# Kernel tuning notes

Hardware: AMD Instinct MI355X
Metric: run time of the kernel (lower is better)

Reference implementation:

```python
import jax, jax.numpy as jnp
import numpy as np

N = 30000
E = 480000
D_IN = 128
EPS = 1e-5
NEG_SLOPE = 0.2
# (in_dim, out_channels, heads) per GATConv layer; concat=True everywhere (PyG default)
CFG = [(D_IN, 100, 5), (500, 50, 5), (250, 32, 4), (128, 8, 4), (32, 1, 1)]
BN_DIMS = (500, 250, 128)


def setup_inputs() -> dict:
    key = jax.random.key(0)
    ks = iter(jax.random.split(key, 80))
    inp = {
        "x": jax.random.normal(next(ks), (N, D_IN), jnp.float32),
        "edge_index": jax.random.randint(next(ks), (2, E), 0, N),
        "edge_weight": jax.random.uniform(next(ks), (E, 1), jnp.float32),
    }
    for l, (cin, cout, h) in enumerate(CFG, 1):
        s = 1.0 / np.sqrt(cin)
        inp[f"W{l}"] = jax.random.normal(next(ks), (cin, h * cout), jnp.float32) * s
        inp[f"a_s{l}"] = jax.random.normal(next(ks), (1, h, cout), jnp.float32) * 0.1
        inp[f"a_d{l}"] = jax.random.normal(next(ks), (1, h, cout), jnp.float32) * 0.1
        inp[f"We{l}"] = jax.random.normal(next(ks), (1, h * cout), jnp.float32)
        inp[f"a_e{l}"] = jax.random.normal(next(ks), (1, h, cout), jnp.float32) * 0.1
        inp[f"b{l}"] = jnp.zeros((h * cout,), jnp.float32)
    for l, d in zip((1, 2, 3), BN_DIMS):
        inp[f"g{l}"] = jnp.ones((d,), jnp.float32)
        inp[f"beta{l}"] = jnp.zeros((d,), jnp.float32)
    return inp


def _gat(x, src, dst, ea, W, a_s, a_d, We, a_e, b, heads, cout):
    """PyG GATConv with edge_dim attention (concat=True)."""
    n = x.shape[0]
    h = (x @ W).reshape(n, heads, cout)            # [N,H,C]
    e = (ea @ We).reshape(-1, heads, cout)         # [E,H,C]
    al_src = (h * a_s).sum(-1)                     # [N,H]
    al_dst = (h * a_d).sum(-1)                     # [N,H]
    logit = jax.nn.leaky_relu(al_src[src] + al_dst[dst] + (e * a_e).sum(-1), NEG_SLOPE)
    m = jax.ops.segment_max(logit, dst, num_segments=n)
    m = jnp.where(jnp.isfinite(m), m, 0.0)
    ex = jnp.exp(logit - m[dst])                   # [E,H]
    den = jax.ops.segment_sum(ex, dst, num_segments=n)
    alpha = ex / jnp.maximum(den[dst], 1e-16)      # segment softmax over in-edges of dst
    out = jax.ops.segment_sum(h[src] * alpha[..., None], dst, num_segments=n)
    return out.reshape(n, heads * cout) + b


def _bn(x, g, b):
    mu = x.mean(0)
    var = x.var(0)  # biased, as torch uses for normalization
    return (x - mu) * jax.lax.rsqrt(var + EPS) * g + b


def reference(x, edge_index, edge_weight,
              W1, a_s1, a_d1, We1, a_e1, b1,
              W2, a_s2, a_d2, We2, a_e2, b2,
              W3, a_s3, a_d3, We3, a_e3, b3,
              W4, a_s4, a_d4, We4, a_e4, b4,
              W5, a_s5, a_d5, We5, a_e5, b5,
              g1, beta1, g2, beta2, g3, beta3):
    # add self loops (PyG default) with edge_attr fill_value='mean'
    loop = jnp.arange(N)
    src = jnp.concatenate([edge_index[0], loop])
    dst = jnp.concatenate([edge_index[1], loop])
    ea = jnp.concatenate([edge_weight, jnp.full((N, 1), edge_weight.mean(), edge_weight.dtype)], axis=0)

    h = _gat(x, src, dst, ea, W1, a_s1, a_d1, We1, a_e1, b1, 5, 100)
    h = jax.nn.relu(_bn(h, g1, beta1))
    h = _gat(h, src, dst, ea, W2, a_s2, a_d2, We2, a_e2, b2, 5, 50)
    h = jax.nn.relu(_bn(h, g2, beta2))
    h = _gat(h, src, dst, ea, W3, a_s3, a_d3, We3, a_e3, b3, 4, 32)
    h = jax.nn.relu(_bn(h, g3, beta3))
    h = _gat(h, src, dst, ea, W4, a_s4, a_d4, We4, a_e4, b4, 4, 8)
    h = jax.nn.relu(h)
    h = _gat(h, src, dst, ea, W5, a_s5, a_d5, We5, a_e5, b5, 1, 1)
    return h
```

## Files before the change

### kernel.cpp

```cpp
#include <hip/hip_runtime.h>
#include <hip/hip_bf16.h>
#include <math.h>

#define NN 30000
#define EE 480000
#define ET (EE + NN)
#define NEG_SLOPE 0.2f
#define BN_EPS 1e-5f

struct LayerCfg { int cin, C, H; };
static const LayerCfg g_cfg[5] = {
    {128, 100, 5}, {500, 50, 5}, {250, 32, 4}, {128, 8, 4}, {32, 1, 1}
};

typedef short short8 __attribute__((ext_vector_type(8)));
typedef float f32x4 __attribute__((ext_vector_type(4)));

__device__ __forceinline__ unsigned short f2bf(float f) {
    unsigned int u = __builtin_bit_cast(unsigned int, f);
    u = (u + 0x7FFFu + ((u >> 16) & 1u)) >> 16;
    return (unsigned short)u;
}
__device__ __forceinline__ float bf2f(unsigned short h) {
    unsigned int u = ((unsigned int)h) << 16;
    return __builtin_bit_cast(float, u);
}


__global__ void ewsum_kernel(const float* __restrict__ ew, float* __restrict__ out) {
    __shared__ float sdata[256];
    int tid = threadIdx.x;
    float s = 0.f;
    for (int i = blockIdx.x * blockDim.x + tid; i < EE; i += gridDim.x * blockDim.x)
        s += ew[i];
    sdata[tid] = s;
    __syncthreads();
    for (int off = 128; off > 0; off >>= 1) {
        if (tid < off) sdata[tid] += sdata[tid + off];
        __syncthreads();
    }
    if (tid == 0) atomicAdd(out, sdata[0]);
}

__global__ void build_edges_kernel(const int* __restrict__ ei,
                                   int* __restrict__ rank, int* __restrict__ cnt) {
    int e = blockIdx.x * blockDim.x + threadIdx.x;
    if (e >= ET) return;
    int d = (e < EE) ? ei[EE + e] : (e - EE);
    rank[e] = atomicAdd(&cnt[d], 1);
}

__global__ void scan_kernel(const int* __restrict__ cnt, int* __restrict__ off) {
    __shared__ int lsum[1024];
    const int T = 1024;
    int t = threadIdx.x;
    int chunk = (NN + T - 1) / T;
    int base = t * chunk;
    int end = min(NN, base + chunk);
    int s = 0;
    for (int i = base; i < end; i++) s += cnt[i];
    lsum[t] = s;
    __syncthreads();
    for (int d = 1; d < T; d <<= 1) {
        int v = (t >= d) ? lsum[t - d] : 0;
        __syncthreads();
        lsum[t] += v;
        __syncthreads();
    }
    int run = (t == 0) ? 0 : lsum[t - 1];
    for (int i = base; i < end; i++) {
        off[i] = run;
        run += cnt[i];
    }
    if (t == 0) off[NN] = ET;
}

__global__ void fill_kernel(const int* __restrict__ ei, const int* __restrict__ rank,
                            const float* __restrict__ ew, const float* __restrict__ esum,
                            const int* __restrict__ off,
                            int* __restrict__ csr_src, float* __restrict__ csr_ea) {
    int e = blockIdx.x * blockDim.x + threadIdx.x;
    if (e >= ET) return;
    int sv, d;
    if (e < EE) { sv = ei[e]; d = ei[EE + e]; }
    else        { sv = e - EE; d = e - EE; }
    int p = off[d] + rank[e];
    csr_src[p] = sv;
    csr_ea[p]  = (e < EE) ? ew[e] : esum[0] * (1.0f / (float)EE);
}


struct PrepArgs {
    const float* W[5];
    const float* We[5];
    const float* ae[5];
    unsigned short* bh[5];
    unsigned short* bl[5];
    float* wedot;
    int K[5], N[5], Kp[5], Np[5], C[5], H[5];
};

__global__ void transpose_all_kernel(PrepArgs a) {
    int l = blockIdx.z;
    if (blockIdx.x == 0 && blockIdx.y == 0 && threadIdx.y == 0 && threadIdx.x < 8) {
        int hd = threadIdx.x;
        if (hd < a.H[l]) {
            int C = a.C[l];
            const float* We = a.We[l] + hd * C;
            const float* ae = a.ae[l] + hd * C;
            float s = 0.f;
            for (int c = 0; c < C; c++) s += We[c] * ae[c];
            a.wedot[l * 8 + hd] = s;
        }
    }
    int Kp = a.Kp[l], Np = a.Np[l], K = a.K[l], N = a.N[l];
    int kb = blockIdx.x * 32, nb = blockIdx.y * 32;
    if (kb >= Kp || nb >= Np) return;
    const float* B = a.W[l];
    unsigned short* Bth = a.bh[l];
    unsigned short* Btl = a.bl[l];
    __shared__ float tile[32][33];
    int tx = threadIdx.x, ty = threadIdx.y;
#pragma unroll
    for (int i = 0; i < 4; i++) {
        int k = kb + ty + i * 8, n = nb + tx;
        tile[ty + i * 8][tx] = (k < K && n < N) ? B[(size_t)k * N + n] : 0.f;
    }
    __syncthreads();
#pragma unroll
    for (int i = 0; i < 4; i++) {
        int n = nb + ty + i * 8, k = kb + tx;
        if (n < Np && k < Kp) {
            float v = tile[tx][ty + i * 8];
            unsigned short hi = f2bf(v);
            unsigned short lo = f2bf(v - bf2f(hi));
            size_t idx = (size_t)n * Kp + k;
            Bth[idx] = hi;
            Btl[idx] = lo;
        }
    }
}

#define GBM 128
#define GBNT 128
#define GBK 32
#define ASTR 36
__global__ __launch_bounds__(256) void gemm_split_kernel(const float* __restrict__ A,
                                                         const unsigned short* __restrict__ Bt_hi,
                                                         const unsigned short* __restrict__ Bt_lo,
                                                         float* __restrict__ Cm,
                                                         unsigned short* __restrict__ Ch16,
                                                         int M, int Kp, int Nc,
                                                         const float* __restrict__ colsum,
                                                         const float* __restrict__ colsumsq,
                                                         const float* __restrict__ g,
                                                         const float* __restrict__ beta,
                                                         int D) {
    __shared__ short AsH[GBM * ASTR];
    __shared__ short AsL[GBM * ASTR];
    __shared__ short BsH[GBNT * ASTR];
    __shared__ short BsL[GBNT * ASTR];
    __shared__ float sscale[512];
    __shared__ float sshift[512];
    int tid = threadIdx.x;
    bool bn = (colsum != nullptr);
    if (bn) {
        for (int c = tid; c < Kp; c += 256) {
            float sc = 0.f, sh = 0.f;
            if (c < D) {
                float mu = colsum[c] * (1.0f / (float)NN);
                float var = colsumsq[c] * (1.0f / (float)NN) - mu * mu;
                sc = g[c] * rsqrtf(var + BN_EPS);
                sh = beta[c] - mu * sc;
            }
            sscale[c] = sc;
            sshift[c] = sh;
        }
        __syncthreads();
    }
    int wave = tid >> 6, lane = tid & 63;
    int q = lane >> 4, r = lane & 15;
    int m0 = blockIdx.y * GBM, n0 = blockIdx.x * GBNT;
    int wm = (wave & 1) * 64, wn = (wave >> 1) * 64;
    f32x4 acc[4][4];
#pragma unroll
    for (int i = 0; i < 4; i++)
#pragma unroll
        for (int j = 0; j < 4; j++) acc[i][j] = (f32x4)(0.f);

    int arow2 = tid >> 1;
    int acol2 = (tid & 1) * 16;
    int brow = tid >> 2;
    int bcol = (tid & 3) * 8;

    int ksteps = Kp / GBK;
    for (int ks = 0; ks < ksteps; ks++) {
        int k0 = ks * GBK;
        {
            int m = m0 + arow2;
            float v[16];
            if (m < M) {
                const float* Ap = A + (size_t)m * Kp + k0 + acol2;
                float4 f0 = *(const float4*)(Ap);
                float4 f1 = *(const float4*)(Ap + 4);
                float4 f2 = *(const float4*)(Ap + 8);
                float4 f3 = *(const float4*)(Ap + 12);
                v[0]=f0.x; v[1]=f0.y; v[2]=f0.z; v[3]=f0.w;
                v[4]=f1.x; v[5]=f1.y; v[6]=f1.z; v[7]=f1.w;
                v[8]=f2.x; v[9]=f2.y; v[10]=f2.z; v[11]=f2.w;
                v[12]=f3.x; v[13]=f3.y; v[14]=f3.z; v[15]=f3.w;
                if (bn) {
                    int cb = k0 + acol2;
#pragma unroll
                    for (int i = 0; i < 16; i++)
                        v[i] = fmaxf(v[i] * sscale[cb + i] + sshift[cb + i], 0.f);
                }
            } else {
#pragma unroll
                for (int i = 0; i < 16; i++) v[i] = 0.f;
            }
#pragma unroll
            for (int i = 0; i < 16; i++) {
                unsigned short hi = f2bf(v[i]);
                unsigned short lo = f2bf(v[i] - bf2f(hi));
                AsH[arow2 * ASTR + acol2 + i] = (short)hi;
                AsL[arow2 * ASTR + acol2 + i] = (short)lo;
            }
        }
#pragma unroll
        for (int p = 0; p < 2; p++) {
            int row = p * 64 + brow;
            size_t gidx = (size_t)(n0 + row) * Kp + k0 + bcol;
            *((uint4*)(BsH + row * ASTR + bcol)) = *((const uint4*)(Bt_hi + gidx));
            *((uint4*)(BsL + row * ASTR + bcol)) = *((const uint4*)(Bt_lo + gidx));
        }
        __syncthreads();
        short8 ah[4], al[4], bh[4], bl[4];
#pragma unroll
        for (int i = 0; i < 4; i++) {
            ah[i] = *((const short8*)(AsH + (wm + i * 16 + r) * ASTR + q * 8));
            al[i] = *((const short8*)(AsL + (wm + i * 16 + r) * ASTR + q * 8));
        }
#pragma unroll
        for (int j = 0; j < 4; j++) {
            bh[j] = *((const short8*)(BsH + (wn + j * 16 + r) * ASTR + q * 8));
            bl[j] = *((const short8*)(BsL + (wn + j * 16 + r) * ASTR + q * 8));
        }
#pragma unroll
        for (int i = 0; i < 4; i++)
#pragma unroll
            for (int j = 0; j < 4; j++) {
                acc[i][j] = __builtin_amdgcn_mfma_f32_16x16x32_bf16(ah[i], bh[j], acc[i][j], 0, 0, 0);
                acc[i][j] = __builtin_amdgcn_mfma_f32_16x16x32_bf16(ah[i], bl[j], acc[i][j], 0, 0, 0);
                acc[i][j] = __builtin_amdgcn_mfma_f32_16x16x32_bf16(al[i], bh[j], acc[i][j], 0, 0, 0);
            }
        __syncthreads();
    }
#pragma unroll
    for (int i = 0; i < 4; i++) {
#pragma unroll
        for (int j = 0; j < 4; j++) {
#pragma unroll
            for (int reg = 0; reg < 4; reg++) {
                int mrow = m0 + wm + i * 16 + q * 4 + reg;
                int ncol = n0 + wn + j * 16 + r;
                if (mrow < M && ncol < Nc) {
                    float val = acc[i][j][reg];
                    if (Cm)   Cm[(size_t)mrow * Nc + ncol] = val;
                    if (Ch16) Ch16[(size_t)mrow * Nc + ncol] = f2bf(val);
                }
            }
        }
    }
}

__global__ void gemv_l5_kernel(const float* __restrict__ X, const float* __restrict__ W,
                               const float* __restrict__ a_s, const float* __restrict__ a_d,
                               float* __restrict__ h, float* __restrict__ al_src,
                               float* __restrict__ al_dst) {
    __shared__ float w[32];
    if (threadIdx.x < 32) w[threadIdx.x] = W[threadIdx.x];
    __syncthreads();
    int n = blockIdx.x * blockDim.x + threadIdx.x;
    if (n >= NN) return;
    const float* row = X + (size_t)n * 32;
    float s = 0.f;
#pragma unroll
    for (int i = 0; i < 8; i++) {
        float4 f = *(const float4*)(row + i * 4);
        s += f.x * w[i * 4] + f.y * w[i * 4 + 1] + f.z * w[i * 4 + 2] + f.w * w[i * 4 + 3];
    }
    h[n] = s;
    al_src[n] = s * a_s[0];
    al_dst[n] = s * a_d[0];
}

__global__ void al_wave_h16_kernel(const unsigned short* __restrict__ h16,
                                   const float* __restrict__ a_s,
                                   const float* __restrict__ a_d,
                                   float* __restrict__ al_src, float* __restrict__ al_dst,
                                   int H, int C, int HC) {
    int w = (blockIdx.x * blockDim.x + threadIdx.x) >> 6;
    int lane = threadIdx.x & 63;
    if (w >= NN) return;
    const unsigned short* row = h16 + (size_t)w * HC;
    float s1[5] = {0.f, 0.f, 0.f, 0.f, 0.f};
    float s2[5] = {0.f, 0.f, 0.f, 0.f, 0.f};
#pragma unroll
    for (int hd = 0; hd < 5; hd++) {
        if (hd >= H) break;
        int base = hd * C;
        for (int c = lane * 2; c < C; c += 128) {
            unsigned int u = *(const unsigned int*)(row + base + c);
            float v0 = bf2f((unsigned short)(u & 0xffffu));
            float v1 = bf2f((unsigned short)(u >> 16));
            s1[hd] += v0 * a_s[base + c] + v1 * a_s[base + c + 1];
            s2[hd] += v0 * a_d[base + c] + v1 * a_d[base + c + 1];
        }
    }
#pragma unroll
    for (int hd = 0; hd < 5; hd++) {
        if (hd >= H) break;
#pragma unroll
        for (int off = 32; off > 0; off >>= 1) {
            s1[hd] += __shfl_xor(s1[hd], off, 64);
            s2[hd] += __shfl_xor(s2[hd], off, 64);
        }
    }
    if (lane == 0) {
#pragma unroll
        for (int hd = 0; hd < 5; hd++) {
            if (hd >= H) break;
            al_src[(size_t)w * H + hd] = s1[hd];
            al_dst[(size_t)w * H + hd] = s2[hd];
        }
    }
}

__global__ void attn_kernel(const float* __restrict__ al_src,
                            const float* __restrict__ al_dst,
                            const int* __restrict__ csr_src,
                            const float* __restrict__ csr_ea,
                            const float* __restrict__ we_dot,
                            const int* __restrict__ off,
                            float* __restrict__ alpha_t, int H, int NH) {
    int t = blockIdx.x * blockDim.x + threadIdx.x;
    if (t >= NH) return;
    int n = t / H, hd = t - n * H;
    int s = off[n], e = off[n + 1];
    float ad = al_dst[(size_t)n * H + hd];
    float wd = we_dot[hd];
    float* arow = alpha_t + (size_t)hd * ET;
    float m = -INFINITY, l = 0.f;
    int p = s;
    for (; p + 3 < e; p += 4) {
        int s0 = csr_src[p], s1 = csr_src[p + 1], s2 = csr_src[p + 2], s3 = csr_src[p + 3];
        float w0 = csr_ea[p], w1 = csr_ea[p + 1], w2 = csr_ea[p + 2], w3 = csr_ea[p + 3];
        float l0 = al_src[(size_t)s0 * H + hd] + ad + w0 * wd;
        float l1 = al_src[(size_t)s1 * H + hd] + ad + w1 * wd;
        float l2 = al_src[(size_t)s2 * H + hd] + ad + w2 * wd;
        float l3 = al_src[(size_t)s3 * H + hd] + ad + w3 * wd;
        l0 = (l0 >= 0.f) ? l0 : NEG_SLOPE * l0;
        l1 = (l1 >= 0.f) ? l1 : NEG_SLOPE * l1;
        l2 = (l2 >= 0.f) ? l2 : NEG_SLOPE * l2;
        l3 = (l3 >= 0.f) ? l3 : NEG_SLOPE * l3;
        arow[p] = l0; arow[p + 1] = l1; arow[p + 2] = l2; arow[p + 3] = l3;
        float mq = fmaxf(fmaxf(l0, l1), fmaxf(l2, l3));
        float nm = fmaxf(m, mq);
        l = l * __expf(m - nm)
          + __expf(l0 - nm) + __expf(l1 - nm) + __expf(l2 - nm) + __expf(l3 - nm);
        m = nm;
    }
    for (; p < e; p++) {
        float lg = al_src[(size_t)csr_src[p] * H + hd] + ad + csr_ea[p] * wd;
        lg = (lg >= 0.f) ? lg : NEG_SLOPE * lg;
        arow[p] = lg;
        float nm = fmaxf(m, lg);
        l = l * __expf(m - nm) + __expf(lg - nm);
        m = nm;
    }
    float inv = 1.f / fmaxf(l, 1e-16f);
    for (p = s; p < e; p++) arow[p] = __expf(arow[p] - m) * inv;
}

__global__ void aggregate_v4h_kernel(const unsigned short* __restrict__ h16,
                                     const float* __restrict__ alpha_t,
                                     const int* __restrict__ off,
                                     const int* __restrict__ csr_src,
                                     const float* __restrict__ bias,
                                     float* __restrict__ out,
                                     int C, int HC, int HC4, int total4, int relu, int opitch) {
    int t = blockIdx.x * blockDim.x + threadIdx.x;
    if (t >= total4) return;
    int n = t / HC4, j4 = t - n * HC4;
    int j = j4 * 4;
    int hd = j / C;
    const float* arow = alpha_t + (size_t)hd * ET;
    int s = off[n], e = off[n + 1];
    float4 acc = make_float4(0.f, 0.f, 0.f, 0.f);
    int p = s;
    for (; p + 3 < e; p += 4) {
        int idx[4]; float a[4];
#pragma unroll
        for (int u = 0; u < 4; u++) { idx[u] = csr_src[p + u]; a[u] = arow[p + u]; }
#pragma unroll
        for (int u = 0; u < 4; u++) {
            ushort4 uv = *(const ushort4*)(h16 + (size_t)idx[u] * HC + j);
            acc.x += a[u] * bf2f(uv.x);
            acc.y += a[u] * bf2f(uv.y);
            acc.z += a[u] * bf2f(uv.z);
            acc.w += a[u] * bf2f(uv.w);
        }
    }
    for (; p < e; p++) {
        int s0 = csr_src[p];
        float a0 = arow[p];
        ushort4 uv = *(const ushort4*)(h16 + (size_t)s0 * HC + j);
        acc.x += a0 * bf2f(uv.x);
        acc.y += a0 * bf2f(uv.y);
        acc.z += a0 * bf2f(uv.z);
        acc.w += a0 * bf2f(uv.w);
    }
    float4 bi = *(const float4*)(bias + j);
    float4 rr = make_float4(acc.x + bi.x, acc.y + bi.y, acc.z + bi.z, acc.w + bi.w);
    if (relu) {
        rr.x = fmaxf(rr.x, 0.f); rr.y = fmaxf(rr.y, 0.f);
        rr.z = fmaxf(rr.z, 0.f); rr.w = fmaxf(rr.w, 0.f);
    }
    *(float4*)(out + (size_t)n * opitch + j) = rr;
}

__global__ void aggregate_v2h_kernel(const unsigned short* __restrict__ h16,
                                     const float* __restrict__ alpha_t,
                                     const int* __restrict__ off,
                                     const int* __restrict__ csr_src,
                                     const float* __restrict__ bias,
                                     float* __restrict__ out,
                                     int C, int HC, int HC2, int total2, int opitch) {
    int t = blockIdx.x * blockDim.x + threadIdx.x;
    if (t >= total2) return;
    int n = t / HC2, j2 = t - n * HC2;
    int j = j2 * 2;
    int hd = j / C;
    const float* arow = alpha_t + (size_t)hd * ET;
    int s = off[n], e = off[n + 1];
    float2 acc = make_float2(0.f, 0.f);
    int p = s;
    for (; p + 3 < e; p += 4) {
        int idx[4]; float a[4];
#pragma unroll
        for (int u = 0; u < 4; u++) { idx[u] = csr_src[p + u]; a[u] = arow[p + u]; }
#pragma unroll
        for (int u = 0; u < 4; u++) {
            ushort2 uv = *(const ushort2*)(h16 + (size_t)idx[u] * HC + j);
            acc.x += a[u] * bf2f(uv.x);
            acc.y += a[u] * bf2f(uv.y);
        }
    }
    for (; p < e; p++) {
        int s0 = csr_src[p];
        float a0 = arow[p];
        ushort2 uv = *(const ushort2*)(h16 + (size_t)s0 * HC + j);
        acc.x += a0 * bf2f(uv.x);
        acc.y += a0 * bf2f(uv.y);
    }
    float2 bi = *(const float2*)(bias + j);
    *(float2*)(out + (size_t)n * opitch + j) = make_float2(acc.x + bi.x, acc.y + bi.y);
}

__global__ void aggregate_kernel(const float* __restrict__ hfeat,
                                 const float* __restrict__ alpha_t,
                                 const int* __restrict__ off, const int* __restrict__ csr_src,
                                 const float* __restrict__ bias, float* __restrict__ out,
                                 int total) {
    int t = blockIdx.x * blockDim.x + threadIdx.x;
    if (t >= total) return;
    int n = t;
    int s = off[n], e = off[n + 1];
    float acc = 0.f;
    int p = s;
    for (; p + 3 < e; p += 4) {
        acc += alpha_t[p] * hfeat[csr_src[p]]
             + alpha_t[p + 1] * hfeat[csr_src[p + 1]]
             + alpha_t[p + 2] * hfeat[csr_src[p + 2]]
             + alpha_t[p + 3] * hfeat[csr_src[p + 3]];
    }
    for (; p < e; p++) acc += alpha_t[p] * hfeat[csr_src[p]];
    out[n] = acc + bias[0];
}


__global__ void bn_stats_kernel(const float* __restrict__ x, float* __restrict__ colsum,
                                float* __restrict__ colsumsq, int D, int pitch) {
    int rows_per_block = (NN + gridDim.x - 1) / gridDim.x;
    int r0 = blockIdx.x * rows_per_block;
    int r1 = min(NN, r0 + rows_per_block);
    int c0 = threadIdx.x;
    int c1 = threadIdx.x + 256;
    float s0 = 0.f, q0 = 0.f, s1 = 0.f, q1 = 0.f;
    for (int r = r0; r < r1; r++) {
        const float* row = x + (size_t)r * pitch;
        if (c0 < D) { float v = row[c0]; s0 += v; q0 += v * v; }
        if (c1 < D) { float v = row[c1]; s1 += v; q1 += v * v; }
    }
    if (c0 < D) { atomicAdd(&colsum[c0], s0); atomicAdd(&colsumsq[c0], q0); }
    if (c1 < D) { atomicAdd(&colsum[c1], s1); atomicAdd(&colsumsq[c1], q1); }
}


static inline size_t align_up(size_t v, size_t a) { return (v + a - 1) / a * a; }

extern "C" void kernel_launch(void* const* d_in, const int* in_sizes, int n_in,
                              void* d_out, int out_size, void* d_ws, size_t ws_size,
                              hipStream_t stream) {
    const float* x_in = (const float*)d_in[0];
    const int* ei     = (const int*)d_in[1];
    const float* ew   = (const float*)d_in[2];

    char* pws = (char*)d_ws;
    size_t off_b = 0;
    auto alloc = [&](size_t bytes) -> void* {
        void* rp = pws + off_b;
        off_b = align_up(off_b + bytes, 256);
        return rp;
    };
    float* B0      = (float*)alloc((size_t)NN * 4);
    float* B1      = (float*)alloc((size_t)NN * 512 * 4);
    unsigned short* H16 = (unsigned short*)alloc((size_t)NN * 500 * 2);
    float* alpha_t = (float*)alloc((size_t)ET * 5 * 4);
    unsigned short* Wt_hi = (unsigned short*)alloc((size_t)600 * 512 * 2);
    unsigned short* Wt_lo = (unsigned short*)alloc((size_t)600 * 512 * 2);
    float* al_src  = (float*)alloc((size_t)NN * 5 * 4);
    float* al_dst  = (float*)alloc((size_t)NN * 5 * 4);
    float* csr_ea  = (float*)alloc((size_t)ET * 4);
    int* rankb     = (int*)alloc((size_t)ET * 4);
    int* csr_src   = (int*)alloc((size_t)ET * 4);
    int* offarr    = (int*)alloc((size_t)(NN + 1) * 4);
    float* we_dot  = (float*)alloc(40 * 4);
    float* esum    = (float*)alloc(4);
    int* cnt       = (int*)alloc((size_t)NN * 4);
    float* colsum_all   = (float*)alloc(3 * 512 * 4);
    float* colsumsq_all = (float*)alloc(3 * 512 * 4);
    char* zero_end = pws + off_b;
    (void)ws_size; (void)n_in; (void)in_sizes; (void)out_size;

    int Kp[5], Np[5];
    size_t wtoff[5];
    size_t acc_off = 0;
    for (int l = 0; l < 5; l++) {
        int K = g_cfg[l].cin, HC = g_cfg[l].C * g_cfg[l].H;
        Kp[l] = (K + 31) / 32 * 32;
        Np[l] = (HC + 127) / 128 * 128;
        wtoff[l] = acc_off;
        acc_off += (size_t)Kp[l] * Np[l];
    }

    PrepArgs pa;
    for (int l = 0; l < 5; l++) {
        pa.W[l]  = (const float*)d_in[3 + l * 6 + 0];
        pa.We[l] = (const float*)d_in[3 + l * 6 + 3];
        pa.ae[l] = (const float*)d_in[3 + l * 6 + 4];
        pa.bh[l] = Wt_hi + wtoff[l];
        pa.bl[l] = Wt_lo + wtoff[l];
        pa.K[l] = g_cfg[l].cin;
        pa.N[l] = g_cfg[l].C * g_cfg[l].H;
        pa.Kp[l] = Kp[l];
        pa.Np[l] = Np[l];
        pa.C[l] = g_cfg[l].C;
        pa.H[l] = g_cfg[l].H;
    }
    pa.wedot = we_dot;

    hipMemsetAsync(esum, 0, (size_t)(zero_end - (char*)esum), stream);
    int ebl = (ET + 255) / 256;
    ewsum_kernel<<<256, 256, 0, stream>>>(ew, esum);
    build_edges_kernel<<<ebl, 256, 0, stream>>>(ei, rankb, cnt);
    scan_kernel<<<1, 1024, 0, stream>>>(cnt, offarr);
    fill_kernel<<<ebl, 256, 0, stream>>>(ei, rankb, ew, esum, offarr, csr_src, csr_ea);

    transpose_all_kernel<<<dim3(16, 16, 5), dim3(32, 8), 0, stream>>>(pa);

    for (int l = 0; l < 5; l++) {
        const LayerCfg& cf = g_cfg[l];
        int H = cf.H, C = cf.C;
        int HC = H * C;
        const float* a_s = (const float*)d_in[3 + l * 6 + 1];
        const float* a_d = (const float*)d_in[3 + l * 6 + 2];
        const float* b   = (const float*)d_in[3 + l * 6 + 5];

        const float* X = (l == 0) ? x_in : B1;
        float* outbuf = (l == 4) ? (float*)d_out : B1;
        int opitch = (l == 4) ? 1 : Kp[l + 1];
        int NH = NN * H;
        int alblocks = (NN * 64 + 255) / 256;

        if (l == 4) {
            gemv_l5_kernel<<<(NN + 255) / 256, 256, 0, stream>>>(
                X, pa.W[4], a_s, a_d, B0, al_src, al_dst);
        } else {
            const float* cs = (l >= 1) ? colsum_all + (l - 1) * 512 : nullptr;
            const float* cq = (l >= 1) ? colsumsq_all + (l - 1) * 512 : nullptr;
            const float* gg = (l >= 1) ? (const float*)d_in[33 + (l - 1) * 2 + 0] : nullptr;
            const float* bb = (l >= 1) ? (const float*)d_in[33 + (l - 1) * 2 + 1] : nullptr;
            int Din = (l >= 1) ? g_cfg[l - 1].C * g_cfg[l - 1].H : 0;
            dim3 ggrid(Np[l] / GBNT, (NN + GBM - 1) / GBM);
            gemm_split_kernel<<<ggrid, 256, 0, stream>>>(X, Wt_hi + wtoff[l], Wt_lo + wtoff[l],
                                                         nullptr, H16,
                                                         NN, Kp[l], HC, cs, cq, gg, bb, Din);
            al_wave_h16_kernel<<<alblocks, 256, 0, stream>>>(H16, a_s, a_d, al_src, al_dst, H, C, HC);
        }

        attn_kernel<<<(NH + 255) / 256, 256, 0, stream>>>(al_src, al_dst, csr_src, csr_ea,
                                                          we_dot + l * 8, offarr, alpha_t, H, NH);

        if (l == 4) {
            aggregate_kernel<<<(NN + 255) / 256, 256, 0, stream>>>(
                B0, alpha_t, offarr, csr_src, b, outbuf, NN);
        } else if ((C & 3) == 0) {
            int HC4 = HC / 4;
            int total4 = NN * HC4;
            aggregate_v4h_kernel<<<(total4 + 255) / 256, 256, 0, stream>>>(
                H16, alpha_t, offarr, csr_src, b, outbuf, C, HC, HC4, total4,
                (l == 3) ? 1 : 0, opitch);
        } else {
            int HC2 = HC / 2;
            int total2 = NN * HC2;
            aggregate_v2h_kernel<<<(total2 + 255) / 256, 256, 0, stream>>>(
                H16, alpha_t, offarr, csr_src, b, outbuf, C, HC, HC2, total2, opitch);
        }

        if (l < 3) {
            bn_stats_kernel<<<512, 256, 0, stream>>>(outbuf, colsum_all + l * 512,
                                                     colsumsq_all + l * 512, HC, opitch);
        }
    }
}
```

Baseline: 826.0 us.

## Pad bf16 feature rows to multiples of 8, vectorize aggregation, fuse prep kernels

Pads the bf16 hidden-feature row pitch to a multiple of 8 so that aggregation can load 16-byte vectors of 8 channels per gathered neighbor. This replaces the separate 4-wide and 2-wide aggregate kernels with one 8-wide kernel that can straddle a head boundary by selecting per-channel alphas. It also merges edge counting, edge-weight summation and weight transpose into one launch to cut launch overhead. The cost is extra padded memory, extra alpha loads per edge, and per-channel select logic in the inner loop. The padded output columns rely on the downstream pitch being large enough to hold them.

Result: no change. 830.6 us (+0.6%).

```diff
diff --git a/kernel.cpp b/kernel.cpp
--- a/kernel.cpp
+++ b/kernel.cpp
@@ -14,6 +14,7 @@
 };
 
 typedef short short8 __attribute__((ext_vector_type(8)));
+typedef unsigned short u16x8 __attribute__((ext_vector_type(8)));
 typedef float f32x4 __attribute__((ext_vector_type(4)));
 
 __device__ __forceinline__ unsigned short f2bf(float f) {
@@ -27,27 +28,87 @@
 }
 
 
-__global__ void ewsum_kernel(const float* __restrict__ ew, float* __restrict__ out) {
+struct PrepArgs {
+    const float* W[5];
+    const float* We[5];
+    const float* ae[5];
+    unsigned short* bh[5];
+    unsigned short* bl[5];
+    float* wedot;
+    int K[5], N[5], Kp[5], Np[5], C[5], H[5];
+};
+
+static const int EBLK = (ET + 255) / 256;
+
+__global__ void prep_fused_kernel(const int* __restrict__ ei, int* __restrict__ rank,
+                                  int* __restrict__ cnt, const float* __restrict__ ew,
+                                  float* __restrict__ esum, PrepArgs a) {
     __shared__ float sdata[256];
+    __shared__ float tile[32][33];
+    int b = blockIdx.x;
     int tid = threadIdx.x;
-    float s = 0.f;
-    for (int i = blockIdx.x * blockDim.x + tid; i < EE; i += gridDim.x * blockDim.x)
-        s += ew[i];
-    sdata[tid] = s;
+
+    if (b < EBLK) {
+        int e = b * 256 + tid;
+        if (e < ET) {
+            int d = (e < EE) ? ei[EE + e] : (e - EE);
+            rank[e] = atomicAdd(&cnt[d], 1);
+        }
+        return;
+    }
+    b -= EBLK;
+    if (b < 256) {
+        float s = 0.f;
+        for (int i = b * 256 + tid; i < EE; i += 65536)
+            s += ew[i];
+        sdata[tid] = s;
+        __syncthreads();
+        for (int off = 128; off > 0; off >>= 1) {
+            if (tid < off) sdata[tid] += sdata[tid + off];
+            __syncthreads();
+        }
+        if (tid == 0) atomicAdd(esum, sdata[0]);
+        return;
+    }
+    b -= 256;
+    int bx = b & 15, by = (b >> 4) & 15, bz = b >> 8;
+    int l = bz;
+    int tx = tid & 31, ty = tid >> 5;
+    if (bx == 0 && by == 0 && ty == 0 && tx < 8) {
+        int hd = tx;
+        if (hd < a.H[l]) {
+            int C = a.C[l];
+            const float* We = a.We[l] + hd * C;
+            const float* ae = a.ae[l] + hd * C;
+            float s = 0.f;
+            for (int c = 0; c < C; c++) s += We[c] * ae[c];
+            a.wedot[l * 8 + hd] = s;
+        }
+    }
+    int Kp = a.Kp[l], Np = a.Np[l], K = a.K[l], N = a.N[l];
+    int kb = bx * 32, nb = by * 32;
+    if (kb >= Kp || nb >= Np) return;
+    const float* B = a.W[l];
+    unsigned short* Bth = a.bh[l];
+    unsigned short* Btl = a.bl[l];
+#pragma unroll
+    for (int i = 0; i < 4; i++) {
+        int k = kb + ty + i * 8, n = nb + tx;
+        tile[ty + i * 8][tx] = (k < K && n < N) ? B[(size_t)k * N + n] : 0.f;
+    }
     __syncthreads();
-    for (int off = 128; off > 0; off >>= 1) {
-        if (tid < off) sdata[tid] += sdata[tid + off];
-        __syncthreads();
-    }
-    if (tid == 0) atomicAdd(out, sdata[0]);
-}
-
-__global__ void build_edges_kernel(const int* __restrict__ ei,
-                                   int* __restrict__ rank, int* __restrict__ cnt) {
-    int e = blockIdx.x * blockDim.x + threadIdx.x;
-    if (e >= ET) return;
-    int d = (e < EE) ? ei[EE + e] : (e - EE);
-    rank[e] = atomicAdd(&cnt[d], 1);
+#pragma unroll
+    for (int i = 0; i < 4; i++) {
+        int n = nb + ty + i * 8, k = kb + tx;
+        if (n < Np && k < Kp) {
+            float v = tile[tx][ty + i * 8];
+            unsigned short hi = f2bf(v);
+            unsigned short lo = f2bf(v - bf2f(hi));
+            size_t idx = (size_t)n * Kp + k;
+            Bth[idx] = hi;
+            Btl[idx] = lo;
+        }
+    }
 }
 
 __global__ void scan_kernel(const int* __restrict__ cnt, int* __restrict__ off) {
@@ -87,58 +148,6 @@
     int p = off[d] + rank[e];
     csr_src[p] = sv;
     csr_ea[p]  = (e < EE) ? ew[e] : esum[0] * (1.0f / (float)EE);
-}
-
-
-struct PrepArgs {
-    const float* W[5];
-    const float* We[5];
-    const float* ae[5];
-    unsigned short* bh[5];
-    unsigned short* bl[5];
-    float* wedot;
-    int K[5], N[5], Kp[5], Np[5], C[5], H[5];
-};
-
-__global__ void transpose_all_kernel(PrepArgs a) {
-    int l = blockIdx.z;
-    if (blockIdx.x == 0 && blockIdx.y == 0 && threadIdx.y == 0 && threadIdx.x < 8) {
-        int hd = threadIdx.x;
-        if (hd < a.H[l]) {
-            int C = a.C[l];
-            const float* We = a.We[l] + hd * C;
-            const float* ae = a.ae[l] + hd * C;
-            float s = 0.f;
-            for (int c = 0; c < C; c++) s += We[c] * ae[c];
-            a.wedot[l * 8 + hd] = s;
-        }
-    }
-    int Kp = a.Kp[l], Np = a.Np[l], K = a.K[l], N = a.N[l];
-    int kb = blockIdx.x * 32, nb = blockIdx.y * 32;
-    if (kb >= Kp || nb >= Np) return;
-    const float* B = a.W[l];
-    unsigned short* Bth = a.bh[l];
-    unsigned short* Btl = a.bl[l];
-    __shared__ float tile[32][33];
-    int tx = threadIdx.x, ty = threadIdx.y;
-#pragma unroll
-    for (int i = 0; i < 4; i++) {
-        int k = kb + ty + i * 8, n = nb + tx;
-        tile[ty + i * 8][tx] = (k < K && n < N) ? B[(size_t)k * N + n] : 0.f;
-    }
-    __syncthreads();
-#pragma unroll
-    for (int i = 0; i < 4; i++) {
-        int n = nb + ty + i * 8, k = kb + tx;
-        if (n < Np && k < Kp) {
-            float v = tile[tx][ty + i * 8];
-            unsigned short hi = f2bf(v);
-            unsigned short lo = f2bf(v - bf2f(hi));
-            size_t idx = (size_t)n * Kp + k;
-            Bth[idx] = hi;
-            Btl[idx] = lo;
-        }
-    }
 }
 
 #define GBM 128
@@ -299,11 +308,11 @@
                                    const float* __restrict__ a_s,
                                    const float* __restrict__ a_d,
                                    float* __restrict__ al_src, float* __restrict__ al_dst,
-                                   int H, int C, int HC) {
+                                   int H, int C, int HCp) {
     int w = (blockIdx.x * blockDim.x + threadIdx.x) >> 6;
     int lane = threadIdx.x & 63;
     if (w >= NN) return;
-    const unsigned short* row = h16 + (size_t)w * HC;
+    const unsigned short* row = h16 + (size_t)w * HCp;
     float s1[5] = {0.f, 0.f, 0.f, 0.f, 0.f};
     float s2[5] = {0.f, 0.f, 0.f, 0.f, 0.f};
 #pragma unroll
@@ -383,89 +392,71 @@
     for (p = s; p < e; p++) arow[p] = __expf(arow[p] - m) * inv;
 }
 
-__global__ void aggregate_v4h_kernel(const unsigned short* __restrict__ h16,
+__global__ void aggregate_v8h_kernel(const unsigned short* __restrict__ h16,
                                      const float* __restrict__ alpha_t,
                                      const int* __restrict__ off,
                                      const int* __restrict__ csr_src,
                                      const float* __restrict__ bias,
                                      float* __restrict__ out,
-                                     int C, int HC, int HC4, int total4, int relu, int opitch) {
+                                     int C, int H, int HC, int hp, int hp8,
+                                     int total8, int relu, int opitch) {
     int t = blockIdx.x * blockDim.x + threadIdx.x;
-    if (t >= total4) return;
-    int n = t / HC4, j4 = t - n * HC4;
-    int j = j4 * 4;
-    int hd = j / C;
-    const float* arow = alpha_t + (size_t)hd * ET;
+    if (t >= total8) return;
+    int n = t / hp8, j8 = t - n * hp8;
+    int j = j8 * 8;
+    int hdA = j / C;
+    int hdB = (j + 7) / C;
+    int bnd = (hdA + 1) * C - j;
+    bnd = (bnd > 8) ? 8 : bnd;
+    float mA = (hdA < H) ? 1.f : 0.f;
+    float mB = (hdB < H) ? 1.f : 0.f;
+    const float* arA = alpha_t + (size_t)((hdA < H) ? hdA : 0) * ET;
+    const float* arB = alpha_t + (size_t)((hdB < H) ? hdB : 0) * ET;
     int s = off[n], e = off[n + 1];
-    float4 acc = make_float4(0.f, 0.f, 0.f, 0.f);
+    const unsigned short* hb = h16 + j;
+    float acc[8];
+#pragma unroll
+    for (int c = 0; c < 8; c++) acc[c] = 0.f;
     int p = s;
     for (; p + 3 < e; p += 4) {
-        int idx[4]; float a[4];
-#pragma unroll
-        for (int u = 0; u < 4; u++) { idx[u] = csr_src[p + u]; a[u] = arow[p + u]; }
+        int idx[4]; float aA[4], aB[4];
 #pragma unroll
         for (int u = 0; u < 4; u++) {
-            ushort4 uv = *(const ushort4*)(h16 + (size_t)idx[u] * HC + j);
-            acc.x += a[u] * bf2f(uv.x);
-            acc.y += a[u] * bf2f(uv.y);
-            acc.z += a[u] * bf2f(uv.z);
-            acc.w += a[u] * bf2f(uv.w);
+            idx[u] = csr_src[p + u];
+            aA[u] = arA[p + u];
+            aB[u] = arB[p + u];
+        }
+#pragma unroll
+        for (int u = 0; u < 4; u++) {
+            u16x8 uv = *(const u16x8*)(hb + (size_t)idx[u] * hp);
+#pragma unroll
+            for (int c = 0; c < 8; c++) {
+                float av = (c < bnd) ? aA[u] : aB[u];
+                acc[c] += av * bf2f(uv[c]);
+            }
         }
     }
     for (; p < e; p++) {
-        int s0 = csr_src[p];
-        float a0 = arow[p];
-        ushort4 uv = *(const ushort4*)(h16 + (size_t)s0 * HC + j);
-        acc.x += a0 * bf2f(uv.x);
-        acc.y += a0 * bf2f(uv.y);
-        acc.z += a0 * bf2f(uv.z);
-        acc.w += a0 * bf2f(uv.w);
-    }
-    float4 bi = *(const float4*)(bias + j);
-    float4 rr = make_float4(acc.x + bi.x, acc.y + bi.y, acc.z + bi.z, acc.w + bi.w);
-    if (relu) {
-        rr.x = fmaxf(rr.x, 0.f); rr.y = fmaxf(rr.y, 0.f);
-        rr.z = fmaxf(rr.z, 0.f); rr.w = fmaxf(rr.w, 0.f);
-    }
-    *(float4*)(out + (size_t)n * opitch + j) = rr;
-}
-
-__global__ void aggregate_v2h_kernel(const unsigned short* __restrict__ h16,
-                                     const float* __restrict__ alpha_t,
-                                     const int* __restrict__ off,
-                                     const int* __restrict__ csr_src,
-                                     const float* __restrict__ bias,
-                                     float* __restrict__ out,
-                                     int C, int HC, int HC2, int total2, int opitch) {
-    int t = blockIdx.x * blockDim.x + threadIdx.x;
-    if (t >= total2) return;
-    int n = t / HC2, j2 = t - n * HC2;
-    int j = j2 * 2;
-    int hd = j / C;
-    const float* arow = alpha_t + (size_t)hd * ET;
-    int s = off[n], e = off[n + 1];
-    float2 acc = make_float2(0.f, 0.f);
-    int p = s;
-    for (; p + 3 < e; p += 4) {
-        int idx[4]; float a[4];
-#pragma unroll
-        for (int u = 0; u < 4; u++) { idx[u] = csr_src[p + u]; a[u] = arow[p + u]; }
-#pragma unroll
-        for (int u = 0; u < 4; u++) {
-            ushort2 uv = *(const ushort2*)(h16 + (size_t)idx[u] * HC + j);
-            acc.x += a[u] * bf2f(uv.x);
-            acc.y += a[u] * bf2f(uv.y);
-        }
-    }
-    for (; p < e; p++) {
-        int s0 = csr_src[p];
-        float a0 = arow[p];
-        ushort2 uv = *(const ushort2*)(h16 + (size_t)s0 * HC + j);
-        acc.x += a0 * bf2f(uv.x);
-        acc.y += a0 * bf2f(uv.y);
-    }
-    float2 bi = *(const float2*)(bias + j);
-    *(float2*)(out + (size_t)n * opitch + j) = make_float2(acc.x + bi.x, acc.y + bi.y);
+        int i0 = csr_src[p];
+        float aA0 = arA[p], aB0 = arB[p];
+        u16x8 uv = *(const u16x8*)(hb + (size_t)i0 * hp);
+#pragma unroll
+        for (int c = 0; c < 8; c++) {
+            float av = (c < bnd) ? aA0 : aB0;
+            acc[c] += av * bf2f(uv[c]);
+        }
+    }
+    float o[8];
+#pragma unroll
+    for (int c = 0; c < 8; c++) {
+        float m = (c < bnd) ? mA : mB;
+        float bi = (j + c < HC) ? bias[j + c] : 0.f;
+        o[c] = acc[c] * m + bi;
+        if (relu) o[c] = fmaxf(o[c], 0.f);
+    }
+    float* op = out + (size_t)n * opitch + j;
+    *(float4*)(op)     = make_float4(o[0], o[1], o[2], o[3]);
+    *(float4*)(op + 4) = make_float4(o[4], o[5], o[6], o[7]);
 }
 
 __global__ void aggregate_kernel(const float* __restrict__ hfeat,
@@ -526,7 +517,7 @@
     };
     float* B0      = (float*)alloc((size_t)NN * 4);
     float* B1      = (float*)alloc((size_t)NN * 512 * 4);
-    unsigned short* H16 = (unsigned short*)alloc((size_t)NN * 500 * 2);
+    unsigned short* H16 = (unsigned short*)alloc((size_t)NN * 504 * 2);
     float* alpha_t = (float*)alloc((size_t)ET * 5 * 4);
     unsigned short* Wt_hi = (unsigned short*)alloc((size_t)600 * 512 * 2);
     unsigned short* Wt_lo = (unsigned short*)alloc((size_t)600 * 512 * 2);
@@ -544,13 +535,14 @@
     char* zero_end = pws + off_b;
     (void)ws_size; (void)n_in; (void)in_sizes; (void)out_size;
 
-    int Kp[5], Np[5];
+    int Kp[5], Np[5], hp[5];
     size_t wtoff[5];
     size_t acc_off = 0;
     for (int l = 0; l < 5; l++) {
         int K = g_cfg[l].cin, HC = g_cfg[l].C * g_cfg[l].H;
         Kp[l] = (K + 31) / 32 * 32;
         Np[l] = (HC + 127) / 128 * 128;
+        hp[l] = (HC + 7) / 8 * 8;
         wtoff[l] = acc_off;
         acc_off += (size_t)Kp[l] * Np[l];
     }
@@ -572,13 +564,10 @@
     pa.wedot = we_dot;
 
     hipMemsetAsync(esum, 0, (size_t)(zero_end - (char*)esum), stream);
-    int ebl = (ET + 255) / 256;
-    ewsum_kernel<<<256, 256, 0, stream>>>(ew, esum);
-    build_edges_kernel<<<ebl, 256, 0, stream>>>(ei, rankb, cnt);
+    int ebl = EBLK;
+    prep_fused_kernel<<<ebl + 256 + 1280, 256, 0, stream>>>(ei, rankb, cnt, ew, esum, pa);
     scan_kernel<<<1, 1024, 0, stream>>>(cnt, offarr);
     fill_kernel<<<ebl, 256, 0, stream>>>(ei, rankb, ew, esum, offarr, csr_src, csr_ea);
-
-    transpose_all_kernel<<<dim3(16, 16, 5), dim3(32, 8), 0, stream>>>(pa);
 
     for (int l = 0; l < 5; l++) {
         const LayerCfg& cf = g_cfg[l];
@@ -606,8 +595,8 @@
             dim3 ggrid(Np[l] / GBNT, (NN + GBM - 1) / GBM);
             gemm_split_kernel<<<ggrid, 256, 0, stream>>>(X, Wt_hi + wtoff[l], Wt_lo + wtoff[l],
                                                          nullptr, H16,
-                                                         NN, Kp[l], HC, cs, cq, gg, bb, Din);
-            al_wave_h16_kernel<<<alblocks, 256, 0, stream>>>(H16, a_s, a_d, al_src, al_dst, H, C, HC);
+                                                         NN, Kp[l], hp[l], cs, cq, gg, bb, Din);
+            al_wave_h16_kernel<<<alblocks, 256, 0, stream>>>(H16, a_s, a_d, al_src, al_dst, H, C, hp[l]);
         }
 
         attn_kernel<<<(NH + 255) / 256, 256, 0, stream>>>(al_src, al_dst, csr_src, csr_ea,
@@ -616,17 +605,12 @@
         if (l == 4) {
             aggregate_kernel<<<(NN + 255) / 256, 256, 0, stream>>>(
                 B0, alpha_t, offarr, csr_src, b, outbuf, NN);
-        } else if ((C & 3) == 0) {
-            int HC4 = HC / 4;
-            int total4 = NN * HC4;
-            aggregate_v4h_kernel<<<(total4 + 255) / 256, 256, 0, stream>>>(
-                H16, alpha_t, offarr, csr_src, b, outbuf, C, HC, HC4, total4,
+        } else {
+            int hp8 = hp[l] / 8;
+            int total8 = NN * hp8;
+            aggregate_v8h_kernel<<<(total8 + 255) / 256, 256, 0, stream>>>(
+                H16, alpha_t, offarr, csr_src, b, outbuf, C, H, HC, hp[l], hp8, total8,
                 (l == 3) ? 1 : 0, opitch);
-        } else {
-            int HC2 = HC / 2;
-            int total2 = NN * HC2;
-            aggregate_v2h_kernel<<<(total2 + 255) / 256, 256, 0, stream>>>(
-                H16, alpha_t, offarr, csr_src, b, outbuf, C, HC, HC2, total2, opitch);
         }
 
         if (l < 3) {
```
